# Kernel tuning notes

Hardware: AMD Instinct MI355X
Metric: run time of the kernel (lower is better)

The kernel has to match this reference:

```python
import jax, jax.numpy as jnp
import numpy as np

S, B, C, H, E = 4096, 2, 256, 8, 131072
CC = C // H


def setup_inputs() -> dict:
    key = jax.random.key(0)
    ks = jax.random.split(key, 12)
    sc = 0.02
    inp = {
        "x": jax.random.normal(ks[0], (S, B, C), jnp.float32),
        "q_id": jax.random.randint(ks[1], (E,), 0, S, jnp.int32),
        "k_id": jax.random.randint(ks[2], (E,), 0, S, jnp.int32),
        "Wq": jax.random.normal(ks[3], (C, C), jnp.float32) * sc,
        "bq": jnp.zeros((C,), jnp.float32),
        "Wk": jax.random.normal(ks[4], (C, C), jnp.float32) * sc,
        "bk": jnp.zeros((C,), jnp.float32),
        "Wv": jax.random.normal(ks[5], (C, C), jnp.float32) * sc,
        "bv": jnp.zeros((C,), jnp.float32),
        "Wx": jax.random.normal(ks[6], (C, C), jnp.float32) * sc,
        "bx": jnp.zeros((C,), jnp.float32),
    }
    return inp


def reference(x, q_id, k_id, Wq, bq, Wk, bk, Wv, bv, Wx, bx):
    s, b, c = x.shape
    cc = c // H
    # qkv projections (torch Linear: x @ W.T + b)
    q = (x @ Wq.T + bq).reshape(s, b, H, cc)
    k = (x @ Wk.T + bk).reshape(s, b, H, cc)
    v = (x @ Wv.T + bv).reshape(s, b, H, cc)
    # per-edge scores: gather along sequence axis by edge ids
    qk = jnp.einsum('ebhc,ebhc->ebh', q[q_id], k[k_id])[..., None]  # [E,b,h,1]
    qk = qk / jnp.sqrt(jnp.asarray(cc, x.dtype))
    eqk = jnp.exp(qk - jnp.max(qk))  # global max, as in original
    # scatter-add softmax normalizer and weighted sum over edges
    d = jnp.zeros((s, b, H, 1), x.dtype).at[q_id].add(eqk)
    out = jnp.zeros((s, b, H, cc), x.dtype).at[q_id].add(eqk * v[k_id])
    out = (out / d).reshape(s, b, c)
    return out @ Wx.T + bx
```

## Files before the change

### kernel.cpp

```cpp
#include <hip/hip_runtime.h>

constexpr int S_  = 4096;
constexpr int B_  = 2;
constexpr int C_  = 256;
constexpr int H_  = 8;
constexpr int E_  = 131072;
constexpr int MR  = S_ * B_;
constexpr int NB  = 512;

typedef __attribute__((ext_vector_type(8))) short bf16x8_t;
typedef __attribute__((ext_vector_type(4))) float f32x4_t;

__device__ __forceinline__ unsigned short f2bf(float f) {
    unsigned int u = __float_as_uint(f);
    u += 0x7fffu + ((u >> 16) & 1u);
    return (unsigned short)(u >> 16);
}
__device__ __forceinline__ float bflo(unsigned int u) { return __uint_as_float(u << 16); }
__device__ __forceinline__ float bfhi(unsigned int u) { return __uint_as_float(u & 0xffff0000u); }

__device__ __forceinline__ void cast8(const float* __restrict__ src, unsigned short* __restrict__ dst, int i) {
    const float4* s = (const float4*)src + (size_t)i * 2;
    float4 a = s[0], b = s[1];
    uint4 o;
    o.x = (unsigned)f2bf(a.x) | ((unsigned)f2bf(a.y) << 16);
    o.y = (unsigned)f2bf(a.z) | ((unsigned)f2bf(a.w) << 16);
    o.z = (unsigned)f2bf(b.x) | ((unsigned)f2bf(b.y) << 16);
    o.w = (unsigned)f2bf(b.z) | ((unsigned)f2bf(b.w) << 16);
    *((uint4*)dst + i) = o;
}

#define BST_REG   0
#define BST_RDY   1
#define BST_XCNT(x)    (16 + (x) * 16)
#define BST_LARR(p, x) (144 + ((p) * 8 + (x)) * 16)
#define BST_GCNT(p)    (656 + (p) * 16)
#define BST_GO(x)      (720 + (x) * 16)
constexpr int BST_INTS = 848;

__device__ __forceinline__ int get_xcc_id() {
    int x;
    asm volatile("s_getreg_b32 %0, hwreg(HW_REG_XCC_ID)" : "=s"(x));
    return x & 7;
}

__device__ __forceinline__ void gbar2(int* bst, int xcd, int xcnt, int ngrp, int ph) {
    __syncthreads();
    if (threadIdx.x == 0) {
        int ret = __hip_atomic_fetch_add(&bst[BST_LARR(ph, xcd)], 1,
                                         __ATOMIC_RELAXED, __HIP_MEMORY_SCOPE_AGENT);
        if (ret == xcnt - 1) {
            __builtin_amdgcn_fence(__ATOMIC_RELEASE, "agent");
            __hip_atomic_fetch_add(&bst[BST_GCNT(ph)], 1,
                                   __ATOMIC_RELAXED, __HIP_MEMORY_SCOPE_AGENT);
            while (__hip_atomic_load(&bst[BST_GCNT(ph)], __ATOMIC_RELAXED,
                                     __HIP_MEMORY_SCOPE_AGENT) < ngrp)
                __builtin_amdgcn_s_sleep(4);
            __builtin_amdgcn_fence(__ATOMIC_ACQUIRE, "agent");
            __hip_atomic_store(&bst[BST_GO(xcd)], ph + 1,
                               __ATOMIC_RELEASE, __HIP_MEMORY_SCOPE_AGENT);
        } else {
            while (__hip_atomic_load(&bst[BST_GO(xcd)], __ATOMIC_RELAXED,
                                     __HIP_MEMORY_SCOPE_AGENT) < ph + 1)
                __builtin_amdgcn_s_sleep(2);
            __builtin_amdgcn_sched_barrier(0);
        }
    }
    __syncthreads();
}

__global__ __launch_bounds__(256, 2) void fused_kernel(
        const float* __restrict__ x, const int* __restrict__ q_id, const int* __restrict__ k_id,
        const float* __restrict__ Wq, const float* __restrict__ bq,
        const float* __restrict__ Wk, const float* __restrict__ bk,
        const float* __restrict__ Wv, const float* __restrict__ bv,
        const float* __restrict__ Wx, const float* __restrict__ bx,
        unsigned short* __restrict__ xb, unsigned short* __restrict__ qb,
        unsigned short* __restrict__ kvb, unsigned short* __restrict__ attnb,
        unsigned short* __restrict__ Wb,
        int* __restrict__ count, int* bst, int* __restrict__ base,
        int* __restrict__ cursor, int* __restrict__ koff,
        float* __restrict__ out) {
    __shared__ __align__(16) unsigned short As[64][264];
    const int bid = blockIdx.x, tid = threadIdx.x;
    const int gid = bid * 256 + tid;
    const int lane = tid & 63, wave = tid >> 6;
    const int l16 = lane & 15, quad = lane >> 4;

    cast8(x, xb, gid);
    cast8(x, xb, gid + 131072);
    if (gid < 32768) {
        int z = gid >> 13, i = gid & 8191;
        const float* src = (z == 0) ? Wq : (z == 1) ? Wk : (z == 2) ? Wv : Wx;
        cast8(src, Wb + (size_t)z * (C_ * C_), i);
    }
    atomicAdd(&count[q_id[gid]], 1);

    __syncthreads();
    int xcd = 0, xcnt = 0, ngrp = 0;
    if (tid == 0) {
        xcd = get_xcc_id();
        __hip_atomic_fetch_add(&bst[BST_XCNT(xcd)], 1, __ATOMIC_RELAXED, __HIP_MEMORY_SCOPE_AGENT);
        int ord = __hip_atomic_fetch_add(&bst[BST_REG], 1, __ATOMIC_RELEASE, __HIP_MEMORY_SCOPE_AGENT);
        if (ord == NB - 1)
            __hip_atomic_store(&bst[BST_RDY], 1, __ATOMIC_RELEASE, __HIP_MEMORY_SCOPE_AGENT);
        while (!__hip_atomic_load(&bst[BST_RDY], __ATOMIC_RELAXED, __HIP_MEMORY_SCOPE_AGENT))
            __builtin_amdgcn_s_sleep(2);
        __builtin_amdgcn_sched_barrier(0);
#pragma unroll
        for (int i = 0; i < 8; ++i) {
            int c = __hip_atomic_load(&bst[BST_XCNT(i)], __ATOMIC_RELAXED, __HIP_MEMORY_SCOPE_AGENT);
            ngrp += (c > 0) ? 1 : 0;
            if (i == xcd) xcnt = c;
        }
    }
    gbar2(bst, xcd, xcnt, ngrp, 0);

    if (bid == 0) {
        const int4* cp = (const int4*)count;
        int4 c0 = cp[tid * 4 + 0], c1 = cp[tid * 4 + 1];
        int4 c2 = cp[tid * 4 + 2], c3 = cp[tid * 4 + 3];
        int tsum = c0.x + c0.y + c0.z + c0.w + c1.x + c1.y + c1.z + c1.w
                 + c2.x + c2.y + c2.z + c2.w + c3.x + c3.y + c3.z + c3.w;
        int incl = tsum;
        const int w = tid >> 6;
#pragma unroll
        for (int off = 1; off < 64; off <<= 1) {
            int y = __shfl_up(incl, off);
            if (lane >= off) incl += y;
        }
        int* wsums = (int*)As;
        if (lane == 63) wsums[w] = incl;
        __syncthreads();
        int ws0 = wsums[0], ws1 = wsums[1], ws2 = wsums[2], ws3 = wsums[3];
        __syncthreads();
        if (tid == 0) base[S_] = ws0 + ws1 + ws2 + ws3;
        int woff = (w > 0 ? ws0 : 0) + (w > 1 ? ws1 : 0) + (w > 2 ? ws2 : 0);
        int run = woff + incl - tsum;
        int idx = tid * 16;
#define EMIT(V) { base[idx] = run; cursor[idx] = run; run += (V); ++idx; }
        EMIT(c0.x) EMIT(c0.y) EMIT(c0.z) EMIT(c0.w)
        EMIT(c1.x) EMIT(c1.y) EMIT(c1.z) EMIT(c1.w)
        EMIT(c2.x) EMIT(c2.y) EMIT(c2.z) EMIT(c2.w)
        EMIT(c3.x) EMIT(c3.y) EMIT(c3.z) EMIT(c3.w)
#undef EMIT
    }
    for (int u = bid; u < 1024; u += NB) {
        const int nb = u & 3, mg = u >> 2;
        const int mbase = mg * 32;
        __syncthreads();
#pragma unroll
        for (int it = 0; it < 4; ++it) {
            int l = it * 256 + tid;
            int r = l >> 5, cc = (l & 31) << 3;
            *(uint4*)&As[r][cc] = *(const uint4*)&xb[(size_t)(mbase + r) * C_ + cc];
        }
        __syncthreads();
        const int colz = (nb << 6) + (wave << 4);
#pragma unroll
        for (int z = 0; z < 3; ++z) {
            const unsigned short* Wrow = Wb + (size_t)z * (C_ * C_) + (size_t)(colz + l16) * C_;
            bf16x8_t breg[8];
#pragma unroll
            for (int ks = 0; ks < 8; ++ks)
                breg[ks] = *(const bf16x8_t*)(Wrow + ks * 32 + quad * 8);
            const float* bias = (z == 0) ? bq : (z == 1) ? bk : bv;
            const float bcol = bias[colz + l16];
#pragma unroll
            for (int mt = 0; mt < 2; ++mt) {
                f32x4_t acc = {0.f, 0.f, 0.f, 0.f};
#pragma unroll
                for (int ks = 0; ks < 8; ++ks) {
                    bf16x8_t a = *(const bf16x8_t*)&As[mt * 16 + l16][ks * 32 + quad * 8];
                    acc = __builtin_amdgcn_mfma_f32_16x16x32_bf16(a, breg[ks], acc, 0, 0, 0);
                }
                const int row0 = mbase + mt * 16 + quad * 4;
                if (z == 0) {
#pragma unroll
                    for (int r = 0; r < 4; ++r)
                        qb[(size_t)(row0 + r) * 256 + colz + l16] = f2bf(acc[r] + bcol);
                } else if (z == 1) {
#pragma unroll
                    for (int r = 0; r < 4; ++r)
                        kvb[(size_t)(row0 + r) * 512 + colz + l16] = f2bf(acc[r] + bcol);
                } else {
#pragma unroll
                    for (int r = 0; r < 4; ++r)
                        kvb[(size_t)(row0 + r) * 512 + 256 + colz + l16] = f2bf(acc[r] + bcol);
                }
            }
        }
    }
    gbar2(bst, xcd, xcnt, ngrp, 1);

    {
        int pos = atomicAdd(&cursor[q_id[gid]], 1);
        koff[pos] = k_id[gid] << 10;
    }
    gbar2(bst, xcd, xcnt, ngrp, 2);

    {
        const int half = lane >> 5, hl = lane & 31;
        const float scale = 0.17677669529663687f;
#pragma unroll
        for (int it = 0; it < 2; ++it) {
            const int s = (bid << 3) + (it << 2) + wave;
            const int e0 = __builtin_amdgcn_readfirstlane(base[s]);
            const int e1 = __builtin_amdgcn_readfirstlane(base[s + 1]);

            const uint4 qq = *((const uint4*)(qb + (size_t)(s * 2 + half) * C_) + hl);
            const float q0 = bflo(qq.x), q1 = bfhi(qq.x), q2 = bflo(qq.y), q3 = bfhi(qq.y);
            const float q4 = bflo(qq.z), q5 = bfhi(qq.z), q6 = bflo(qq.w), q7 = bfhi(qq.w);

            float a0 = 0.f, a1 = 0.f, a2 = 0.f, a3 = 0.f;
            float a4 = 0.f, a5 = 0.f, a6 = 0.f, a7 = 0.f;
            float wsum = 0.f;

            auto edge = [&](const uint4& kk, const uint4& vv) {
                float p = q0 * bflo(kk.x) + q1 * bfhi(kk.x)
                        + q2 * bflo(kk.y) + q3 * bfhi(kk.y)
                        + q4 * bflo(kk.z) + q5 * bfhi(kk.z)
                        + q6 * bflo(kk.w) + q7 * bfhi(kk.w);
                p += __shfl_xor(p, 1);
                p += __shfl_xor(p, 2);
                const float w = __expf(p * scale);
                a0 = fmaf(w, bflo(vv.x), a0); a1 = fmaf(w, bfhi(vv.x), a1);
                a2 = fmaf(w, bflo(vv.y), a2); a3 = fmaf(w, bfhi(vv.y), a3);
                a4 = fmaf(w, bflo(vv.z), a4); a5 = fmaf(w, bfhi(vv.z), a5);
                a6 = fmaf(w, bflo(vv.w), a6); a7 = fmaf(w, bfhi(vv.w), a7);
                wsum += w;
            };
            auto fetch = [&](int my, int t, uint4& kk, uint4& vv) {
                int o = __builtin_amdgcn_readlane(my, t);
                const uint4* p = (const uint4*)(kvb + o + half * 512);
                kk = p[hl]; vv = p[32 + hl];
            };

            for (int b0 = e0; b0 < e1; b0 += 64) {
                const int m = min(64, e1 - b0);
                const int my = koff[b0 + ((lane < m) ? lane : 0)];
                uint4 k0 = {}, v0 = {}, k1 = {}, v1 = {};
                uint4 k2 = {}, v2 = {}, k3 = {}, v3 = {};
                if (m > 0) fetch(my, 0, k0, v0);
                if (m > 1) fetch(my, 1, k1, v1);
                if (m > 2) fetch(my, 2, k2, v2);
                if (m > 3) fetch(my, 3, k3, v3);
                int t = 0;
                for (; t + 7 < m; t += 4) {
                    edge(k0, v0); fetch(my, t + 4, k0, v0);
                    edge(k1, v1); fetch(my, t + 5, k1, v1);
                    edge(k2, v2); fetch(my, t + 6, k2, v2);
                    edge(k3, v3); fetch(my, t + 7, k3, v3);
                }
                const int rem = m - t;
                if (rem > 0) { edge(k0, v0); if (rem > 4) fetch(my, t + 4, k0, v0); }
                if (rem > 1) { edge(k1, v1); if (rem > 5) fetch(my, t + 5, k1, v1); }
                if (rem > 2) { edge(k2, v2); if (rem > 6) fetch(my, t + 6, k2, v2); }
                if (rem > 3) edge(k3, v3);
                if (rem > 4) edge(k0, v0);
                if (rem > 5) edge(k1, v1);
                if (rem > 6) edge(k2, v2);
            }

            const float inv = 1.0f / wsum;
            uint4 o;
            o.x = (unsigned)f2bf(a0 * inv) | ((unsigned)f2bf(a1 * inv) << 16);
            o.y = (unsigned)f2bf(a2 * inv) | ((unsigned)f2bf(a3 * inv) << 16);
            o.z = (unsigned)f2bf(a4 * inv) | ((unsigned)f2bf(a5 * inv) << 16);
            o.w = (unsigned)f2bf(a6 * inv) | ((unsigned)f2bf(a7 * inv) << 16);
            *((uint4*)(attnb + (size_t)(s * 2 + half) * C_) + hl) = o;
        }
    }
    gbar2(bst, xcd, xcnt, ngrp, 3);

    {
        const int nbp = bid & 3, mgp = bid >> 2;
        const int mbase = mgp * 64;
#pragma unroll
        for (int it = 0; it < 8; ++it) {
            int l = it * 256 + tid;
            int r = l >> 5, cc = (l & 31) << 3;
            *(uint4*)&As[r][cc] = *(const uint4*)&attnb[(size_t)(mbase + r) * C_ + cc];
        }
        __syncthreads();
        const int colz = (nbp << 6) + (wave << 4);
        const unsigned short* Wrow = Wb + (size_t)3 * (C_ * C_) + (size_t)(colz + l16) * C_;
        bf16x8_t breg[8];
#pragma unroll
        for (int ks = 0; ks < 8; ++ks)
            breg[ks] = *(const bf16x8_t*)(Wrow + ks * 32 + quad * 8);
        const float bcol = bx[colz + l16];
#pragma unroll
        for (int mt = 0; mt < 4; ++mt) {
            f32x4_t acc = {0.f, 0.f, 0.f, 0.f};
#pragma unroll
            for (int ks = 0; ks < 8; ++ks) {
                bf16x8_t a = *(const bf16x8_t*)&As[mt * 16 + l16][ks * 32 + quad * 8];
                acc = __builtin_amdgcn_mfma_f32_16x16x32_bf16(a, breg[ks], acc, 0, 0, 0);
            }
            const int row0 = mbase + mt * 16 + quad * 4;
#pragma unroll
            for (int r = 0; r < 4; ++r)
                out[(size_t)(row0 + r) * C_ + colz + l16] = acc[r] + bcol;
        }
    }
}


extern "C" void kernel_launch(void* const* d_in, const int* in_sizes, int n_in,
                              void* d_out, int out_size, void* d_ws, size_t ws_size,
                              hipStream_t stream) {
    const float* x  = (const float*)d_in[0];
    const int* q_id = (const int*)d_in[1];
    const int* k_id = (const int*)d_in[2];
    const float* Wq = (const float*)d_in[3];
    const float* bq = (const float*)d_in[4];
    const float* Wk = (const float*)d_in[5];
    const float* bk = (const float*)d_in[6];
    const float* Wv = (const float*)d_in[7];
    const float* bv = (const float*)d_in[8];
    const float* Wx = (const float*)d_in[9];
    const float* bx = (const float*)d_in[10];
    float* out = (float*)d_out;

    char* ws = (char*)d_ws;
    unsigned short* xb    = (unsigned short*)ws;   ws += (size_t)MR * C_ * 2;
    unsigned short* qb    = (unsigned short*)ws;   ws += (size_t)MR * C_ * 2;
    unsigned short* kvb   = (unsigned short*)ws;   ws += (size_t)MR * 512 * 2;
    unsigned short* attnb = (unsigned short*)ws;   ws += (size_t)MR * C_ * 2;
    unsigned short* Wb    = (unsigned short*)ws;   ws += (size_t)4 * C_ * C_ * 2;
    int* count = (int*)ws;                         ws += S_ * 4;
    int* bst   = (int*)ws;                         ws += BST_INTS * 4;
    int* base  = (int*)ws;                         ws += (S_ + 1) * 4;
    int* cursor = (int*)ws;                        ws += S_ * 4;
    int* koff_sorted = (int*)ws;

    hipMemsetAsync(count, 0, (S_ + BST_INTS) * sizeof(int), stream);
    fused_kernel<<<NB, 256, 0, stream>>>(x, q_id, k_id, Wq, bq, Wk, bk, Wv, bv, Wx, bx,
                                         xb, qb, kvb, attnb, Wb,
                                         count, bst, base, cursor, koff_sorted, out);
}
```

Measured before the change: 176.8 us.

## Split persistent kernel into three launches and parallelize edge aggregation across waves

The single persistent kernel is split into three launches: projection plus edge bucketing, edge attention, and output projection. This replaces the last two software grid barriers with kernel boundaries. Edges are now bucketed by (q, k-half) so that gathers for each segment stay in one half of the KV buffer for locality. Each query row is processed by two waves splitting its edges, with partial sums reduced through shared memory, which raises parallelism (2048 blocks) at the cost of extra launch overhead and a reduction step.

```diff
diff --git a/kernel.cpp b/kernel.cpp
--- a/kernel.cpp
+++ b/kernel.cpp
@@ -69,23 +69,31 @@
     __syncthreads();
 }
 
-__global__ __launch_bounds__(256, 2) void fused_kernel(
+
+__global__ __launch_bounds__(256, 2) void fusedA(
         const float* __restrict__ x, const int* __restrict__ q_id, const int* __restrict__ k_id,
         const float* __restrict__ Wq, const float* __restrict__ bq,
         const float* __restrict__ Wk, const float* __restrict__ bk,
         const float* __restrict__ Wv, const float* __restrict__ bv,
-        const float* __restrict__ Wx, const float* __restrict__ bx,
+        const float* __restrict__ Wx,
         unsigned short* __restrict__ xb, unsigned short* __restrict__ qb,
-        unsigned short* __restrict__ kvb, unsigned short* __restrict__ attnb,
-        unsigned short* __restrict__ Wb,
+        unsigned short* __restrict__ kvb, unsigned short* __restrict__ Wb,
         int* __restrict__ count, int* bst, int* __restrict__ base,
-        int* __restrict__ cursor, int* __restrict__ koff,
-        float* __restrict__ out) {
-    __shared__ __align__(16) unsigned short As[64][264];
+        int* __restrict__ cursor, int* __restrict__ koff) {
+    __shared__ __align__(16) unsigned short As[32][264];
     const int bid = blockIdx.x, tid = threadIdx.x;
     const int gid = bid * 256 + tid;
     const int lane = tid & 63, wave = tid >> 6;
     const int l16 = lane & 15, quad = lane >> 4;
+
+    int xcd = 0;
+    if (tid == 0) {
+        xcd = get_xcc_id();
+        __hip_atomic_fetch_add(&bst[BST_XCNT(xcd)], 1, __ATOMIC_RELAXED, __HIP_MEMORY_SCOPE_AGENT);
+        int ord = __hip_atomic_fetch_add(&bst[BST_REG], 1, __ATOMIC_RELEASE, __HIP_MEMORY_SCOPE_AGENT);
+        if (ord == NB - 1)
+            __hip_atomic_store(&bst[BST_RDY], 1, __ATOMIC_RELEASE, __HIP_MEMORY_SCOPE_AGENT);
+    }
 
     cast8(x, xb, gid);
     cast8(x, xb, gid + 131072);
@@ -94,16 +102,14 @@
         const float* src = (z == 0) ? Wq : (z == 1) ? Wk : (z == 2) ? Wv : Wx;
         cast8(src, Wb + (size_t)z * (C_ * C_), i);
     }
-    atomicAdd(&count[q_id[gid]], 1);
-
-    __syncthreads();
-    int xcd = 0, xcnt = 0, ngrp = 0;
+    {
+        int q = q_id[gid], k = k_id[gid];
+        atomicAdd(&count[q + ((k >> 11) << 12)], 1);
+    }
+
+    __syncthreads();
+    int xcnt = 0, ngrp = 0;
     if (tid == 0) {
-        xcd = get_xcc_id();
-        __hip_atomic_fetch_add(&bst[BST_XCNT(xcd)], 1, __ATOMIC_RELAXED, __HIP_MEMORY_SCOPE_AGENT);
-        int ord = __hip_atomic_fetch_add(&bst[BST_REG], 1, __ATOMIC_RELEASE, __HIP_MEMORY_SCOPE_AGENT);
-        if (ord == NB - 1)
-            __hip_atomic_store(&bst[BST_RDY], 1, __ATOMIC_RELEASE, __HIP_MEMORY_SCOPE_AGENT);
         while (!__hip_atomic_load(&bst[BST_RDY], __ATOMIC_RELAXED, __HIP_MEMORY_SCOPE_AGENT))
             __builtin_amdgcn_s_sleep(2);
         __builtin_amdgcn_sched_barrier(0);
@@ -118,10 +124,12 @@
 
     if (bid == 0) {
         const int4* cp = (const int4*)count;
-        int4 c0 = cp[tid * 4 + 0], c1 = cp[tid * 4 + 1];
-        int4 c2 = cp[tid * 4 + 2], c3 = cp[tid * 4 + 3];
-        int tsum = c0.x + c0.y + c0.z + c0.w + c1.x + c1.y + c1.z + c1.w
-                 + c2.x + c2.y + c2.z + c2.w + c3.x + c3.y + c3.z + c3.w;
+        int4 c[8];
+#pragma unroll
+        for (int j = 0; j < 8; ++j) c[j] = cp[tid * 8 + j];
+        int tsum = 0;
+#pragma unroll
+        for (int j = 0; j < 8; ++j) tsum += c[j].x + c[j].y + c[j].z + c[j].w;
         int incl = tsum;
         const int w = tid >> 6;
 #pragma unroll
@@ -134,15 +142,15 @@
         __syncthreads();
         int ws0 = wsums[0], ws1 = wsums[1], ws2 = wsums[2], ws3 = wsums[3];
         __syncthreads();
-        if (tid == 0) base[S_] = ws0 + ws1 + ws2 + ws3;
+        if (tid == 0) base[2 * S_] = E_;
         int woff = (w > 0 ? ws0 : 0) + (w > 1 ? ws1 : 0) + (w > 2 ? ws2 : 0);
         int run = woff + incl - tsum;
-        int idx = tid * 16;
+        int idx = tid * 32;
 #define EMIT(V) { base[idx] = run; cursor[idx] = run; run += (V); ++idx; }
-        EMIT(c0.x) EMIT(c0.y) EMIT(c0.z) EMIT(c0.w)
-        EMIT(c1.x) EMIT(c1.y) EMIT(c1.z) EMIT(c1.w)
-        EMIT(c2.x) EMIT(c2.y) EMIT(c2.z) EMIT(c2.w)
-        EMIT(c3.x) EMIT(c3.y) EMIT(c3.z) EMIT(c3.w)
+#pragma unroll
+        for (int j = 0; j < 8; ++j) {
+            EMIT(c[j].x) EMIT(c[j].y) EMIT(c[j].z) EMIT(c[j].w)
+        }
 #undef EMIT
     }
     for (int u = bid; u < 1024; u += NB) {
@@ -194,115 +202,143 @@
     gbar2(bst, xcd, xcnt, ngrp, 1);
 
     {
-        int pos = atomicAdd(&cursor[q_id[gid]], 1);
-        koff[pos] = k_id[gid] << 10;
-    }
-    gbar2(bst, xcd, xcnt, ngrp, 2);
-
-    {
-        const int half = lane >> 5, hl = lane & 31;
-        const float scale = 0.17677669529663687f;
-#pragma unroll
-        for (int it = 0; it < 2; ++it) {
-            const int s = (bid << 3) + (it << 2) + wave;
-            const int e0 = __builtin_amdgcn_readfirstlane(base[s]);
-            const int e1 = __builtin_amdgcn_readfirstlane(base[s + 1]);
-
-            const uint4 qq = *((const uint4*)(qb + (size_t)(s * 2 + half) * C_) + hl);
-            const float q0 = bflo(qq.x), q1 = bfhi(qq.x), q2 = bflo(qq.y), q3 = bfhi(qq.y);
-            const float q4 = bflo(qq.z), q5 = bfhi(qq.z), q6 = bflo(qq.w), q7 = bfhi(qq.w);
-
-            float a0 = 0.f, a1 = 0.f, a2 = 0.f, a3 = 0.f;
-            float a4 = 0.f, a5 = 0.f, a6 = 0.f, a7 = 0.f;
-            float wsum = 0.f;
-
-            auto edge = [&](const uint4& kk, const uint4& vv) {
-                float p = q0 * bflo(kk.x) + q1 * bfhi(kk.x)
-                        + q2 * bflo(kk.y) + q3 * bfhi(kk.y)
-                        + q4 * bflo(kk.z) + q5 * bfhi(kk.z)
-                        + q6 * bflo(kk.w) + q7 * bfhi(kk.w);
-                p += __shfl_xor(p, 1);
-                p += __shfl_xor(p, 2);
-                const float w = __expf(p * scale);
-                a0 = fmaf(w, bflo(vv.x), a0); a1 = fmaf(w, bfhi(vv.x), a1);
-                a2 = fmaf(w, bflo(vv.y), a2); a3 = fmaf(w, bfhi(vv.y), a3);
-                a4 = fmaf(w, bflo(vv.z), a4); a5 = fmaf(w, bfhi(vv.z), a5);
-                a6 = fmaf(w, bflo(vv.w), a6); a7 = fmaf(w, bfhi(vv.w), a7);
-                wsum += w;
-            };
-            auto fetch = [&](int my, int t, uint4& kk, uint4& vv) {
-                int o = __builtin_amdgcn_readlane(my, t);
-                const uint4* p = (const uint4*)(kvb + o + half * 512);
-                kk = p[hl]; vv = p[32 + hl];
-            };
-
-            for (int b0 = e0; b0 < e1; b0 += 64) {
-                const int m = min(64, e1 - b0);
-                const int my = koff[b0 + ((lane < m) ? lane : 0)];
-                uint4 k0 = {}, v0 = {}, k1 = {}, v1 = {};
-                uint4 k2 = {}, v2 = {}, k3 = {}, v3 = {};
-                if (m > 0) fetch(my, 0, k0, v0);
-                if (m > 1) fetch(my, 1, k1, v1);
-                if (m > 2) fetch(my, 2, k2, v2);
-                if (m > 3) fetch(my, 3, k3, v3);
-                int t = 0;
-                for (; t + 7 < m; t += 4) {
-                    edge(k0, v0); fetch(my, t + 4, k0, v0);
-                    edge(k1, v1); fetch(my, t + 5, k1, v1);
-                    edge(k2, v2); fetch(my, t + 6, k2, v2);
-                    edge(k3, v3); fetch(my, t + 7, k3, v3);
-                }
-                const int rem = m - t;
-                if (rem > 0) { edge(k0, v0); if (rem > 4) fetch(my, t + 4, k0, v0); }
-                if (rem > 1) { edge(k1, v1); if (rem > 5) fetch(my, t + 5, k1, v1); }
-                if (rem > 2) { edge(k2, v2); if (rem > 6) fetch(my, t + 6, k2, v2); }
-                if (rem > 3) edge(k3, v3);
-                if (rem > 4) edge(k0, v0);
-                if (rem > 5) edge(k1, v1);
-                if (rem > 6) edge(k2, v2);
+        int q = q_id[gid], k = k_id[gid];
+        int pos = atomicAdd(&cursor[q + ((k >> 11) << 12)], 1);
+        koff[pos] = k << 10;
+    }
+}
+
+
+__global__ __launch_bounds__(256) void attn_edge(
+        const unsigned short* __restrict__ qb, const unsigned short* __restrict__ kvb,
+        const int* __restrict__ base, const int* __restrict__ koff,
+        unsigned short* __restrict__ attnb) {
+    __shared__ float red[2][64][9];
+    const int lane = threadIdx.x & 63;
+    const int wave = threadIdx.x >> 6;
+    const int rw = wave >> 1, part = wave & 1;
+    const int s = blockIdx.x * 2 + rw;
+    const int half = lane >> 5, hl = lane & 31;
+
+    const uint4 qq = *((const uint4*)(qb + (size_t)(s * 2 + half) * C_) + hl);
+    const float q0 = bflo(qq.x), q1 = bfhi(qq.x), q2 = bflo(qq.y), q3 = bfhi(qq.y);
+    const float q4 = bflo(qq.z), q5 = bfhi(qq.z), q6 = bflo(qq.w), q7 = bfhi(qq.w);
+
+    float a0 = 0.f, a1 = 0.f, a2 = 0.f, a3 = 0.f, a4 = 0.f, a5 = 0.f, a6 = 0.f, a7 = 0.f;
+    float wsum = 0.f;
+    const float scale = 0.17677669529663687f;
+
+    auto edge = [&](const uint4& kk, const uint4& vv) {
+        float p = q0 * bflo(kk.x) + q1 * bfhi(kk.x)
+                + q2 * bflo(kk.y) + q3 * bfhi(kk.y)
+                + q4 * bflo(kk.z) + q5 * bfhi(kk.z)
+                + q6 * bflo(kk.w) + q7 * bfhi(kk.w);
+        p += __shfl_xor(p, 1);
+        p += __shfl_xor(p, 2);
+        const float w = __expf(p * scale);
+        a0 = fmaf(w, bflo(vv.x), a0); a1 = fmaf(w, bfhi(vv.x), a1);
+        a2 = fmaf(w, bflo(vv.y), a2); a3 = fmaf(w, bfhi(vv.y), a3);
+        a4 = fmaf(w, bflo(vv.z), a4); a5 = fmaf(w, bfhi(vv.z), a5);
+        a6 = fmaf(w, bflo(vv.w), a6); a7 = fmaf(w, bfhi(vv.w), a7);
+        wsum += w;
+    };
+    auto fetch = [&](int my, int t, uint4& kk, uint4& vv) {
+        int o = __builtin_amdgcn_readlane(my, part + 2 * t);
+        const uint4* p = (const uint4*)(kvb + o + half * 512);
+        kk = p[hl]; vv = p[32 + hl];
+    };
+
+#pragma unroll
+    for (int seg = 0; seg < 2; ++seg) {
+        const int cb = seg * S_ + s;
+        const int e0 = __builtin_amdgcn_readfirstlane(base[cb]);
+        const int e1 = __builtin_amdgcn_readfirstlane(base[cb + 1]);
+        for (int b0 = e0; b0 < e1; b0 += 64) {
+            const int m = min(64, e1 - b0);
+            const int my = koff[b0 + ((lane < m) ? lane : 0)];
+            const int nm = (m > part) ? ((m - part + 1) >> 1) : 0;
+            uint4 k0 = {}, v0 = {}, k1 = {}, v1 = {};
+            uint4 k2 = {}, v2 = {}, k3 = {}, v3 = {};
+            if (nm > 0) fetch(my, 0, k0, v0);
+            if (nm > 1) fetch(my, 1, k1, v1);
+            if (nm > 2) fetch(my, 2, k2, v2);
+            if (nm > 3) fetch(my, 3, k3, v3);
+            int t = 0;
+            for (; t + 7 < nm; t += 4) {
+                edge(k0, v0); fetch(my, t + 4, k0, v0);
+                edge(k1, v1); fetch(my, t + 5, k1, v1);
+                edge(k2, v2); fetch(my, t + 6, k2, v2);
+                edge(k3, v3); fetch(my, t + 7, k3, v3);
             }
-
-            const float inv = 1.0f / wsum;
-            uint4 o;
-            o.x = (unsigned)f2bf(a0 * inv) | ((unsigned)f2bf(a1 * inv) << 16);
-            o.y = (unsigned)f2bf(a2 * inv) | ((unsigned)f2bf(a3 * inv) << 16);
-            o.z = (unsigned)f2bf(a4 * inv) | ((unsigned)f2bf(a5 * inv) << 16);
-            o.w = (unsigned)f2bf(a6 * inv) | ((unsigned)f2bf(a7 * inv) << 16);
-            *((uint4*)(attnb + (size_t)(s * 2 + half) * C_) + hl) = o;
-        }
-    }
-    gbar2(bst, xcd, xcnt, ngrp, 3);
-
-    {
-        const int nbp = bid & 3, mgp = bid >> 2;
-        const int mbase = mgp * 64;
-#pragma unroll
-        for (int it = 0; it < 8; ++it) {
-            int l = it * 256 + tid;
-            int r = l >> 5, cc = (l & 31) << 3;
-            *(uint4*)&As[r][cc] = *(const uint4*)&attnb[(size_t)(mbase + r) * C_ + cc];
-        }
-        __syncthreads();
-        const int colz = (nbp << 6) + (wave << 4);
-        const unsigned short* Wrow = Wb + (size_t)3 * (C_ * C_) + (size_t)(colz + l16) * C_;
-        bf16x8_t breg[8];
-#pragma unroll
-        for (int ks = 0; ks < 8; ++ks)
-            breg[ks] = *(const bf16x8_t*)(Wrow + ks * 32 + quad * 8);
-        const float bcol = bx[colz + l16];
-#pragma unroll
-        for (int mt = 0; mt < 4; ++mt) {
-            f32x4_t acc = {0.f, 0.f, 0.f, 0.f};
-#pragma unroll
-            for (int ks = 0; ks < 8; ++ks) {
-                bf16x8_t a = *(const bf16x8_t*)&As[mt * 16 + l16][ks * 32 + quad * 8];
-                acc = __builtin_amdgcn_mfma_f32_16x16x32_bf16(a, breg[ks], acc, 0, 0, 0);
-            }
-            const int row0 = mbase + mt * 16 + quad * 4;
-#pragma unroll
-            for (int r = 0; r < 4; ++r)
-                out[(size_t)(row0 + r) * C_ + colz + l16] = acc[r] + bcol;
-        }
+            const int rem = nm - t;
+            if (rem > 0) { edge(k0, v0); if (rem > 4) fetch(my, t + 4, k0, v0); }
+            if (rem > 1) { edge(k1, v1); if (rem > 5) fetch(my, t + 5, k1, v1); }
+            if (rem > 2) { edge(k2, v2); if (rem > 6) fetch(my, t + 6, k2, v2); }
+            if (rem > 3) edge(k3, v3);
+            if (rem > 4) edge(k0, v0);
+            if (rem > 5) edge(k1, v1);
+            if (rem > 6) edge(k2, v2);
+        }
+    }
+
+    if (part == 1) {
+        float* r = red[rw][lane];
+        r[0] = a0; r[1] = a1; r[2] = a2; r[3] = a3;
+        r[4] = a4; r[5] = a5; r[6] = a6; r[7] = a7; r[8] = wsum;
+    }
+    __syncthreads();
+    if (part == 0) {
+        const float* r = red[rw][lane];
+        a0 += r[0]; a1 += r[1]; a2 += r[2]; a3 += r[3];
+        a4 += r[4]; a5 += r[5]; a6 += r[6]; a7 += r[7]; wsum += r[8];
+        const float inv = 1.0f / wsum;
+        uint4 o;
+        o.x = (unsigned)f2bf(a0 * inv) | ((unsigned)f2bf(a1 * inv) << 16);
+        o.y = (unsigned)f2bf(a2 * inv) | ((unsigned)f2bf(a3 * inv) << 16);
+        o.z = (unsigned)f2bf(a4 * inv) | ((unsigned)f2bf(a5 * inv) << 16);
+        o.w = (unsigned)f2bf(a6 * inv) | ((unsigned)f2bf(a7 * inv) << 16);
+        *((uint4*)(attnb + (size_t)(s * 2 + half) * C_) + hl) = o;
+    }
+}
+
+
+__global__ __launch_bounds__(256) void gemm_proj(
+        const unsigned short* __restrict__ attnb, const unsigned short* __restrict__ Wxb,
+        const float* __restrict__ bx, float* __restrict__ out) {
+    __shared__ __align__(16) unsigned short As[64][264];
+    const int tid = threadIdx.x;
+    const int nb = blockIdx.x & 3, mg = blockIdx.x >> 2;
+    const int lane = tid & 63, wave = tid >> 6;
+    const int l16 = lane & 15, quad = lane >> 4;
+    const int colz = (nb << 6) + (wave << 4);
+
+    const unsigned short* Wrow = Wxb + (size_t)(colz + l16) * C_;
+    bf16x8_t breg[8];
+#pragma unroll
+    for (int ks = 0; ks < 8; ++ks)
+        breg[ks] = *(const bf16x8_t*)(Wrow + ks * 32 + quad * 8);
+    const float bcol = bx[colz + l16];
+
+    const int mbase = mg * 64;
+#pragma unroll
+    for (int it = 0; it < 8; ++it) {
+        int l = it * 256 + tid;
+        int r = l >> 5, cc = (l & 31) << 3;
+        *(uint4*)&As[r][cc] = *(const uint4*)&attnb[(size_t)(mbase + r) * C_ + cc];
+    }
+    __syncthreads();
+#pragma unroll
+    for (int mt = 0; mt < 4; ++mt) {
+        f32x4_t acc = {0.f, 0.f, 0.f, 0.f};
+#pragma unroll
+        for (int ks = 0; ks < 8; ++ks) {
+            bf16x8_t a = *(const bf16x8_t*)&As[mt * 16 + l16][ks * 32 + quad * 8];
+            acc = __builtin_amdgcn_mfma_f32_16x16x32_bf16(a, breg[ks], acc, 0, 0, 0);
+        }
+        const int row0 = mbase + mt * 16 + quad * 4;
+#pragma unroll
+        for (int r = 0; r < 4; ++r)
+            out[(size_t)(row0 + r) * C_ + colz + l16] = acc[r] + bcol;
     }
 }
 
@@ -329,14 +365,15 @@
     unsigned short* kvb   = (unsigned short*)ws;   ws += (size_t)MR * 512 * 2;
     unsigned short* attnb = (unsigned short*)ws;   ws += (size_t)MR * C_ * 2;
     unsigned short* Wb    = (unsigned short*)ws;   ws += (size_t)4 * C_ * C_ * 2;
-    int* count = (int*)ws;                         ws += S_ * 4;
+    int* count = (int*)ws;                         ws += 2 * S_ * 4;
     int* bst   = (int*)ws;                         ws += BST_INTS * 4;
-    int* base  = (int*)ws;                         ws += (S_ + 1) * 4;
-    int* cursor = (int*)ws;                        ws += S_ * 4;
+    int* base  = (int*)ws;                         ws += (2 * S_ + 1) * 4;
+    int* cursor = (int*)ws;                        ws += 2 * S_ * 4;
     int* koff_sorted = (int*)ws;
 
-    hipMemsetAsync(count, 0, (S_ + BST_INTS) * sizeof(int), stream);
-    fused_kernel<<<NB, 256, 0, stream>>>(x, q_id, k_id, Wq, bq, Wk, bk, Wv, bv, Wx, bx,
-                                         xb, qb, kvb, attnb, Wb,
-                                         count, bst, base, cursor, koff_sorted, out);
-}
+    hipMemsetAsync(count, 0, (2 * S_ + BST_INTS) * sizeof(int), stream);
+    fusedA<<<NB, 256, 0, stream>>>(x, q_id, k_id, Wq, bq, Wk, bk, Wv, bv, Wx,
+                                   xb, qb, kvb, Wb, count, bst, base, cursor, koff_sorted);
+    attn_edge<<<S_ / 2, 256, 0, stream>>>(qb, kvb, base, koff_sorted, attnb);
+    gemm_proj<<<512, 256, 0, stream>>>(attnb, Wb + (size_t)3 * C_ * C_, bx, out);
+}
```

Measured after the change: 162.4 us. -8.2%, faster.
